# Optimization experiments

Measured on AMD Instinct MI355X. Metric: run time of the kernel, lower is better.

## Reference

```python
import jax, jax.numpy as jnp
import numpy as np

N = 21  # nodes per graph (20 laser sectors + 1 robot node)
MAX_RANGE = 10.0
_bound = np.linspace(-np.pi / 2 - 0.03, np.pi / 2, 21, dtype=np.float32)[:-1]
_angles = _bound + np.float32(np.pi / 20)
ANGLE_FEAT = jnp.asarray(np.stack([np.sin(_angles), np.cos(_angles)], 1), dtype=jnp.float32)  # [20,2]


def _build_nodes(state24):
    # state24: [B,24] -> node features [B,21,7]
    B = state24.shape[0]
    laser = state24[:, :20, None] / MAX_RANGE                       # [B,20,1]
    angle = jnp.broadcast_to(ANGLE_FEAT[None], (B, 20, 2))          # [B,20,2]
    sector = jnp.concatenate([laser, angle, jnp.zeros((B, 20, 4), state24.dtype)], -1)  # [B,20,7]
    robot = jnp.concatenate([jnp.zeros((B, 1, 3), state24.dtype), state24[:, None, 20:]], -1)  # [B,1,7]
    return jnp.concatenate([sector, robot], axis=1)                 # [B,21,7]


def _gatv2(x, Wl, Wr, att, bias, heads, dim):
    # GATv2 over a fully-connected graph with self-loops (dense all-pairs).
    # e_ij = att . leaky_relu(Wl x_j + Wr x_i); alpha = softmax_j; out_i = sum_j alpha_ij (Wl x_j)
    B = x.shape[0]
    gl = (x @ Wl).reshape(B, N, heads, dim)  # source transform [B,j,H,D]
    gr = (x @ Wr).reshape(B, N, heads, dim)  # target transform [B,i,H,D]
    s = jax.nn.leaky_relu(gl[:, None] + gr[:, :, None], negative_slope=0.2)  # [B,i,j,H,D]
    e = jnp.einsum('bijhd,hd->bijh', s, att)                                  # [B,i,j,H]
    alpha = jax.nn.softmax(e, axis=2)                                          # softmax over sources j
    out = jnp.einsum('bijh,bjhd->bihd', alpha, gl).reshape(B, N, heads * dim)
    return out + bias


def setup_inputs() -> dict:
    key = jax.random.key(0)
    ks = jax.random.split(key, 16)
    r = lambda k, shape, s: (jax.random.normal(k, shape, dtype=jnp.float32) * s)
    B = 1024
    return {
        'state24': jax.random.normal(ks[0], (B, 24), dtype=jnp.float32),
        'Wl1': r(ks[1], (7, 256), 0.3), 'Wr1': r(ks[2], (7, 256), 0.3),
        'att1': r(ks[3], (4, 64), 0.1), 'b1': r(ks[4], (256,), 0.02),
        'Wl2': r(ks[5], (256, 64), 0.06), 'Wr2': r(ks[6], (256, 64), 0.06),
        'att2': r(ks[7], (1, 64), 0.1), 'b2': r(ks[8], (64,), 0.02),
        'fc1_w': r(ks[9], (64, 256), 0.12), 'fc1_b': r(ks[10], (256,), 0.02),
        'fc2_w': r(ks[11], (256, 256), 0.06), 'fc2_b': r(ks[12], (256,), 0.02),
        'fc3_w': r(ks[13], (256, 2), 0.06), 'fc3_b': r(ks[14], (2,), 0.02),
    }


def reference(state24, Wl1, Wr1, att1, b1, Wl2, Wr2, att2, b2,
              fc1_w, fc1_b, fc2_w, fc2_b, fc3_w, fc3_b):
    x = _build_nodes(state24)                               # [B,21,7]
    h = jax.nn.elu(_gatv2(x, Wl1, Wr1, att1, b1, 4, 64))    # [B,21,256]
    h = _gatv2(h, Wl2, Wr2, att2, b2, 1, 64)                # [B,21,64]
    nfv = jnp.mean(h, axis=1)                               # global_mean_pool -> [B,64]
    h = jax.nn.relu(nfv @ fc1_w + fc1_b)
    h = jax.nn.relu(h @ fc2_w + fc2_b)
    return jnp.tanh(h @ fc3_w + fc3_b)                      # [B,2]
```

## Files before the change

### kernel.cpp

```cpp
#include <hip/hip_runtime.h>
#include <hip/hip_fp16.h>
#include <math.h>

#define PI_D 3.141592653589793

typedef _Float16 h2 __attribute__((ext_vector_type(2)));
typedef _Float16 h4 __attribute__((ext_vector_type(4)));
typedef _Float16 h8 __attribute__((ext_vector_type(8)));
typedef unsigned short us8 __attribute__((ext_vector_type(8)));
typedef __fp16 f16v2 __attribute__((ext_vector_type(2)));

#define STR1 264
#define STR1H 132
#define STR1O 33
#define STR2 66

static __device__ __forceinline__ h2 pack_h2(float a, float b) {
    return __builtin_bit_cast(h2, __builtin_amdgcn_cvt_pkrtz(a, b));
}

static __device__ __forceinline__ float fdot2(h2 a, h2 b, float c) {
    return __builtin_amdgcn_fdot2(__builtin_bit_cast(f16v2, a),
                                  __builtin_bit_cast(f16v2, b), c, false);
}

static __device__ __forceinline__ h8 habs8(h8 x) {
    us8 u = __builtin_bit_cast(us8, x);
    us8 m = {0x7fff, 0x7fff, 0x7fff, 0x7fff, 0x7fff, 0x7fff, 0x7fff, 0x7fff};
    return __builtin_bit_cast(h8, (us8)(u & m));
}

__global__ __launch_bounds__(256, 4) void actor_fused_kernel(
    const float* __restrict__ state24,
    const float* __restrict__ Wl1, const float* __restrict__ Wr1,
    const float* __restrict__ att1, const float* __restrict__ b1,
    const float* __restrict__ Wl2, const float* __restrict__ Wr2,
    const float* __restrict__ att2, const float* __restrict__ b2,
    const float* __restrict__ fc1_w, const float* __restrict__ fc1_b,
    const float* __restrict__ fc2_w, const float* __restrict__ fc2_b,
    const float* __restrict__ fc3_w, const float* __restrict__ fc3_b,
    float* __restrict__ out, int B)
{
    const int bix = blockIdx.x;
    if (bix >= B) return;
    const int tid = threadIdx.x;

    __shared__ float sinL[20], cosL[20], laserL[20], robotL[4];
    __shared__ __align__(16) h2 attLh[128];
    __shared__ __align__(16) float att2L[64];
    __shared__ __align__(16) _Float16 gr1h[24 * STR1];
    __shared__ __align__(16) union {
        struct { _Float16 gl1h[21 * STR1]; float eP[1764]; float uv[168]; } p1;
        struct { float gl2[24 * STR2]; float gr2[24 * STR2]; float e2[504];
                 float red[4][256]; float nfv[64]; float ha[256]; float hb[256]; } p2;
    } U;

    if (tid < 20) {
        double step = (PI_D + 0.03) / 20.0;
        float bound = (float)(-PI_D / 2.0 - 0.03 + (double)tid * step);
        float ang = bound + (float)(PI_D / 20.0);
        sinL[tid] = sinf(ang);
        cosL[tid] = cosf(ang);
        laserL[tid] = state24[bix * 24 + tid] * 0.1f;
    }
    if (tid >= 32 && tid < 36) robotL[tid - 32] = state24[bix * 24 + 20 + (tid - 32)];
    if (tid < 128) {
        float2 ap = ((const float2*)att1)[tid];
        attLh[tid] = pack_h2(ap.x, ap.y);
    }
    if (tid < 64) att2L[tid] = att2[tid];
    __syncthreads();

    {
        float wl[7], wr[7];
        #pragma unroll
        for (int k = 0; k < 7; k++) { wl[k] = Wl1[k * 256 + tid]; wr[k] = Wr1[k * 256 + tid]; }
        #pragma unroll
        for (int n = 0; n < 20; n++) {
            float l = laserL[n], s = sinL[n], c = cosL[n];
            U.p1.gl1h[n * STR1 + tid] = (_Float16)(l * wl[0] + s * wl[1] + c * wl[2]);
            gr1h[n * STR1 + tid]     = (_Float16)(l * wr[0] + s * wr[1] + c * wr[2]);
        }
        float r0 = robotL[0], r1 = robotL[1], r2 = robotL[2], r3 = robotL[3];
        U.p1.gl1h[20 * STR1 + tid] = (_Float16)(r0 * wl[3] + r1 * wl[4] + r2 * wl[5] + r3 * wl[6]);
        gr1h[20 * STR1 + tid]     = (_Float16)(r0 * wr[3] + r1 * wr[4] + r2 * wr[5] + r3 * wr[6]);
    }
    __syncthreads();

    if (tid < 168) {
        int r = tid < 84 ? tid : tid - 84;
        int h = r / 21, idx = r - h * 21;
        const _Float16* rowp = (tid < 84 ? U.p1.gl1h : gr1h) + idx * STR1 + h * 64;
        const h8* row8 = (const h8*)rowp;
        const h2* ar = attLh + h * 32;
        float l0 = 0.f, l1 = 0.f;
        #pragma unroll
        for (int ch = 0; ch < 8; ++ch) {
            h8 g = row8[ch];
            l0 = fdot2(__builtin_shufflevector(g, g, 0, 1), ar[ch * 4 + 0], l0);
            l1 = fdot2(__builtin_shufflevector(g, g, 2, 3), ar[ch * 4 + 1], l1);
            l0 = fdot2(__builtin_shufflevector(g, g, 4, 5), ar[ch * 4 + 2], l0);
            l1 = fdot2(__builtin_shufflevector(g, g, 6, 7), ar[ch * 4 + 3], l1);
        }
        U.p1.uv[tid] = l0 + l1;
    }
    __syncthreads();

    {
        const int h = tid >> 6;
        const int lane = tid & 63;
        h2 ar[32];
        #pragma unroll
        for (int q = 0; q < 32; ++q) ar[q] = attLh[h * 32 + q];
        const float* uvU = U.p1.uv + h * 21;
        const float* uvV = U.p1.uv + 84 + h * 21;

        for (int it = 0; it < 7; ++it) {
            int q = it * 64 + lane;
            if (q < 441) {
                int i = q / 21;
                int j = q - i * 21;
                const h8* gA8 = (const h8*)(U.p1.gl1h + j * STR1 + h * 64);
                const h8* gB8 = (const h8*)(gr1h + i * STR1 + h * 64);
                float m0 = 0.f, m1 = 0.f;
                #pragma unroll
                for (int ch = 0; ch < 8; ++ch) {
                    h8 x = gA8[ch] + gB8[ch];
                    h8 ax = habs8(x);
                    m0 = fdot2(__builtin_shufflevector(ax, ax, 0, 1), ar[ch * 4 + 0], m0);
                    m1 = fdot2(__builtin_shufflevector(ax, ax, 2, 3), ar[ch * 4 + 1], m1);
                    m0 = fdot2(__builtin_shufflevector(ax, ax, 4, 5), ar[ch * 4 + 2], m0);
                    m1 = fdot2(__builtin_shufflevector(ax, ax, 6, 7), ar[ch * 4 + 3], m1);
                }
                U.p1.eP[h * 441 + q] = 0.6f * (uvU[j] + uvV[i]) + 0.4f * (m0 + m1);
            }
        }
    }
    __syncthreads();

    if (tid < 84) {
        float* row = U.p1.eP + tid * 21;
        float m = row[0];
        #pragma unroll
        for (int j = 1; j < 21; j++) m = fmaxf(m, row[j]);
        float s = 0.f;
        #pragma unroll
        for (int j = 0; j < 21; j++) { float v = __expf(row[j] - m); row[j] = v; s += v; }
        float r = 1.f / s;
        #pragma unroll
        for (int j = 0; j < 21; j++) row[j] *= r;
    }
    __syncthreads();

    {
        h2 zz = {(_Float16)0.f, (_Float16)0.f};
        for (int z = tid; z < 384; z += 256)
            ((h2*)gr1h)[(21 + (z >> 7)) * STR1H + (z & 127)] = zz;

        int p = tid & 127, gi = tid >> 7;
        int h = p >> 5;
        float2 bb = ((const float2*)b1)[p];
        const h2* gcol = (const h2*)U.p1.gl1h + p;
        for (int i = gi; i < 21; i += 2) {
            const float* al = U.p1.eP + (h * 21 + i) * 21;
            float a0 = 0.f, a1 = 0.f;
            #pragma unroll
            for (int j = 0; j < 21; ++j) {
                float alpha = al[j];
                h2 gv = gcol[j * STR1H];
                a0 = fmaf(alpha, (float)gv.x, a0);
                a1 = fmaf(alpha, (float)gv.y, a1);
            }
            float v0 = a0 + bb.x, v1 = a1 + bb.y;
            v0 = v0 > 0.f ? v0 : __expf(v0) - 1.f;
            v1 = v1 > 0.f ? v1 : __expf(v1) - 1.f;
            h2 o; o.x = (_Float16)v0; o.y = (_Float16)v1;
            ((h2*)gr1h)[i * STR1H + p] = o;
        }
    }
    __syncthreads();

    {
        int c = tid & 63, g = tid >> 6;
        float accL[6] = {0, 0, 0, 0, 0, 0}, accR[6] = {0, 0, 0, 0, 0, 0};
        const h8* hrow8 = (const h8*)gr1h;
        const float* pwl = Wl2 + c;
        const float* pwr = Wr2 + c;
        for (int ch = 0; ch < 32; ++ch) {
            float wlv[8], wrv[8];
            #pragma unroll
            for (int r = 0; r < 8; ++r) {
                wlv[r] = pwl[(8 * ch + r) * 64];
                wrv[r] = pwr[(8 * ch + r) * 64];
            }
            h2 wlA = pack_h2(wlv[0], wlv[1]), wlB = pack_h2(wlv[2], wlv[3]);
            h2 wlC = pack_h2(wlv[4], wlv[5]), wlD = pack_h2(wlv[6], wlv[7]);
            h2 wrA = pack_h2(wrv[0], wrv[1]), wrB = pack_h2(wrv[2], wrv[3]);
            h2 wrC = pack_h2(wrv[4], wrv[5]), wrD = pack_h2(wrv[6], wrv[7]);
            #pragma unroll
            for (int m = 0; m < 6; ++m) {
                int n = g + 4 * m;
                h8 hv = hrow8[n * STR1O + ch];
                h2 s0 = __builtin_shufflevector(hv, hv, 0, 1);
                h2 s1 = __builtin_shufflevector(hv, hv, 2, 3);
                h2 s2 = __builtin_shufflevector(hv, hv, 4, 5);
                h2 s3 = __builtin_shufflevector(hv, hv, 6, 7);
                accL[m] = fdot2(s0, wlA, accL[m]);
                accL[m] = fdot2(s1, wlB, accL[m]);
                accL[m] = fdot2(s2, wlC, accL[m]);
                accL[m] = fdot2(s3, wlD, accL[m]);
                accR[m] = fdot2(s0, wrA, accR[m]);
                accR[m] = fdot2(s1, wrB, accR[m]);
                accR[m] = fdot2(s2, wrC, accR[m]);
                accR[m] = fdot2(s3, wrD, accR[m]);
            }
        }
        #pragma unroll
        for (int m = 0; m < 6; ++m) {
            int n = g + 4 * m;
            U.p2.gl2[n * STR2 + c] = accL[m];
            U.p2.gr2[n * STR2 + c] = accR[m];
        }
    }
    __syncthreads();

    for (int it = 0; it < 2; ++it) {
        int t = it * 256 + tid;
        if (t < 441) {
            int i = t / 21;
            int j = t - i * 21;
            const float2* gA = (const float2*)(U.p2.gl2 + j * STR2);
            const float2* gB = (const float2*)(U.p2.gr2 + i * STR2);
            const float2* aa = (const float2*)att2L;
            float l0 = 0.f, l1 = 0.f, m0 = 0.f, m1 = 0.f;
            #pragma unroll
            for (int dp = 0; dp < 32; ++dp) {
                float2 va = gA[dp], vb = gB[dp], a = aa[dp];
                float x0 = va.x + vb.x, x1 = va.y + vb.y;
                l0 = fmaf(a.x, x0, l0); m0 = fmaf(a.x, fabsf(x0), m0);
                l1 = fmaf(a.y, x1, l1); m1 = fmaf(a.y, fabsf(x1), m1);
            }
            U.p2.e2[t] = 0.6f * (l0 + l1) + 0.4f * (m0 + m1);
        }
    }
    __syncthreads();

    if (tid < 24) {
        float* row = U.p2.e2 + tid * 21;
        if (tid < 21) {
            float m = row[0];
            #pragma unroll
            for (int j = 1; j < 21; j++) m = fmaxf(m, row[j]);
            float s = 0.f;
            #pragma unroll
            for (int j = 0; j < 21; j++) { float v = __expf(row[j] - m); row[j] = v; s += v; }
            float r = 1.f / s;
            #pragma unroll
            for (int j = 0; j < 21; j++) row[j] *= r;
        } else {
            #pragma unroll
            for (int j = 0; j < 21; j++) row[j] = 0.f;
        }
    }
    __syncthreads();

    {
        int d = tid & 63, g = tid >> 6;
        float sacc = 0.f;
        #pragma unroll
        for (int m = 0; m < 6; ++m) {
            int i = g + 4 * m;
            const float* al = U.p2.e2 + i * 21;
            float acc = 0.f;
            #pragma unroll
            for (int j = 0; j < 21; ++j) acc = fmaf(al[j], U.p2.gl2[j * STR2 + d], acc);
            sacc += acc;
        }
        U.p2.red[g][d] = sacc;
    }
    __syncthreads();
    if (tid < 64) {
        U.p2.nfv[tid] = (U.p2.red[0][tid] + U.p2.red[1][tid] + U.p2.red[2][tid] + U.p2.red[3][tid])
                        * (1.f / 21.f) + b2[tid];
    }
    __syncthreads();

    {
        int c = tid & 63, g = tid >> 6;
        const float4* w4 = (const float4*)fc1_w;
        float4 acc = {0.f, 0.f, 0.f, 0.f};
        #pragma unroll
        for (int kk = 0; kk < 16; ++kk) {
            int k = g * 16 + kk;
            float xv = U.p2.nfv[k];
            float4 w = w4[k * 64 + c];
            acc.x = fmaf(xv, w.x, acc.x);
            acc.y = fmaf(xv, w.y, acc.y);
            acc.z = fmaf(xv, w.z, acc.z);
            acc.w = fmaf(xv, w.w, acc.w);
        }
        ((float4*)U.p2.red[g])[c] = acc;
    }
    __syncthreads();
    {
        float v = U.p2.red[0][tid] + U.p2.red[1][tid] + U.p2.red[2][tid] + U.p2.red[3][tid]
                  + fc1_b[tid];
        U.p2.ha[tid] = fmaxf(v, 0.f);
    }
    __syncthreads();

    {
        int c = tid & 63, g = tid >> 6;
        const float4* w4 = (const float4*)fc2_w;
        float4 acc = {0.f, 0.f, 0.f, 0.f};
        #pragma unroll 8
        for (int kk = 0; kk < 64; ++kk) {
            int k = g * 64 + kk;
            float xv = U.p2.ha[k];
            float4 w = w4[k * 64 + c];
            acc.x = fmaf(xv, w.x, acc.x);
            acc.y = fmaf(xv, w.y, acc.y);
            acc.z = fmaf(xv, w.z, acc.z);
            acc.w = fmaf(xv, w.w, acc.w);
        }
        ((float4*)U.p2.red[g])[c] = acc;
    }
    __syncthreads();
    {
        float v = U.p2.red[0][tid] + U.p2.red[1][tid] + U.p2.red[2][tid] + U.p2.red[3][tid]
                  + fc2_b[tid];
        U.p2.hb[tid] = fmaxf(v, 0.f);
    }
    __syncthreads();

    if (tid < 128) {
        int o = tid >> 6, l = tid & 63;
        float s = 0.f;
        #pragma unroll
        for (int m = 0; m < 4; m++) { int k = l + 64 * m; s = fmaf(U.p2.hb[k], fc3_w[k * 2 + o], s); }
        #pragma unroll
        for (int off = 32; off >= 1; off >>= 1) s += __shfl_down(s, off, 64);
        if (l == 0) out[bix * 2 + o] = tanhf(s + fc3_b[o]);
    }
}

extern "C" void kernel_launch(void* const* d_in, const int* in_sizes, int n_in,
                              void* d_out, int out_size, void* d_ws, size_t ws_size,
                              hipStream_t stream) {
    const float* state24 = (const float*)d_in[0];
    const float* Wl1 = (const float*)d_in[1];
    const float* Wr1 = (const float*)d_in[2];
    const float* att1 = (const float*)d_in[3];
    const float* b1 = (const float*)d_in[4];
    const float* Wl2 = (const float*)d_in[5];
    const float* Wr2 = (const float*)d_in[6];
    const float* att2 = (const float*)d_in[7];
    const float* b2 = (const float*)d_in[8];
    const float* fc1_w = (const float*)d_in[9];
    const float* fc1_b = (const float*)d_in[10];
    const float* fc2_w = (const float*)d_in[11];
    const float* fc2_b = (const float*)d_in[12];
    const float* fc3_w = (const float*)d_in[13];
    const float* fc3_b = (const float*)d_in[14];
    float* out = (float*)d_out;

    int B = in_sizes[0] / 24;
    actor_fused_kernel<<<B, 256, 0, stream>>>(
        state24, Wl1, Wr1, att1, b1, Wl2, Wr2, att2, b2,
        fc1_w, fc1_b, fc2_w, fc2_b, fc3_w, fc3_b, out, B);
}
```

Before: 134.2 us.

## Prepack layer-2 and FC weights to fp16 and rework layer-1 aggregation

Adds a small pre-kernel that converts Wl2/Wr2 and fc1/fc2 weights to fp16 in a packed h8 layout in workspace. Each of the 1024 blocks can then load them with vector loads and use fdot2, instead of gathering strided fp32 values and packing them per block. The FC hidden activations are also stored in fp16. The layer-1 aggregation is restructured so each thread keeps one column of gl in registers and reads padded attention rows as float4. The cost is an extra launch and reduced precision in the FC layers.

```diff
diff --git a/kernel.cpp b/kernel.cpp
--- a/kernel.cpp
+++ b/kernel.cpp
@@ -5,15 +5,14 @@
 #define PI_D 3.141592653589793
 
 typedef _Float16 h2 __attribute__((ext_vector_type(2)));
-typedef _Float16 h4 __attribute__((ext_vector_type(4)));
 typedef _Float16 h8 __attribute__((ext_vector_type(8)));
 typedef unsigned short us8 __attribute__((ext_vector_type(8)));
 typedef __fp16 f16v2 __attribute__((ext_vector_type(2)));
 
 #define STR1 264
-#define STR1H 132
 #define STR1O 33
 #define STR2 66
+#define EPS 24
 
 static __device__ __forceinline__ h2 pack_h2(float a, float b) {
     return __builtin_bit_cast(h2, __builtin_amdgcn_cvt_pkrtz(a, b));
@@ -30,15 +29,52 @@
     return __builtin_bit_cast(h8, (us8)(u & m));
 }
 
+__global__ __launch_bounds__(256) void pack_weights_kernel(
+    const float* __restrict__ Wl2, const float* __restrict__ Wr2,
+    const float* __restrict__ fc1_w, const float* __restrict__ fc2_w,
+    h8* __restrict__ ws)
+{
+    int idx = blockIdx.x * 256 + threadIdx.x;
+    if (idx < 4096) {
+        const float* W = idx < 2048 ? Wl2 : Wr2;
+        int t = idx & 2047;
+        int ch = t >> 6, c = t & 63;
+        h8 o;
+        #pragma unroll
+        for (int r = 0; r < 8; ++r) o[r] = (_Float16)W[(8 * ch + r) * 64 + c];
+        ws[idx] = o;
+    } else if (idx < 6144) {
+        int t = idx - 4096;
+        int k2 = t >> 6, c = t & 63;
+        h8 o;
+        #pragma unroll
+        for (int q = 0; q < 4; ++q) {
+            o[2 * q]     = (_Float16)fc1_w[(2 * k2) * 256 + 4 * c + q];
+            o[2 * q + 1] = (_Float16)fc1_w[(2 * k2 + 1) * 256 + 4 * c + q];
+        }
+        ws[idx] = o;
+    } else {
+        int t = idx - 6144;
+        int k2 = t >> 6, c = t & 63;
+        h8 o;
+        #pragma unroll
+        for (int q = 0; q < 4; ++q) {
+            o[2 * q]     = (_Float16)fc2_w[(2 * k2) * 256 + 4 * c + q];
+            o[2 * q + 1] = (_Float16)fc2_w[(2 * k2 + 1) * 256 + 4 * c + q];
+        }
+        ws[idx] = o;
+    }
+}
+
 __global__ __launch_bounds__(256, 4) void actor_fused_kernel(
     const float* __restrict__ state24,
     const float* __restrict__ Wl1, const float* __restrict__ Wr1,
     const float* __restrict__ att1, const float* __restrict__ b1,
-    const float* __restrict__ Wl2, const float* __restrict__ Wr2,
     const float* __restrict__ att2, const float* __restrict__ b2,
-    const float* __restrict__ fc1_w, const float* __restrict__ fc1_b,
-    const float* __restrict__ fc2_w, const float* __restrict__ fc2_b,
+    const float* __restrict__ fc1_b, const float* __restrict__ fc2_b,
     const float* __restrict__ fc3_w, const float* __restrict__ fc3_b,
+    const h8* __restrict__ wsL, const h8* __restrict__ wsR,
+    const h8* __restrict__ wsF1, const h8* __restrict__ wsF2,
     float* __restrict__ out, int B)
 {
     const int bix = blockIdx.x;
@@ -50,9 +86,12 @@
     __shared__ __align__(16) float att2L[64];
     __shared__ __align__(16) _Float16 gr1h[24 * STR1];
     __shared__ __align__(16) union {
-        struct { _Float16 gl1h[21 * STR1]; float eP[1764]; float uv[168]; } p1;
+        struct { _Float16 gl1h[21 * STR1];
+                 float eP[84 * EPS];
+                 float uv[168]; } p1;
         struct { float gl2[24 * STR2]; float gr2[24 * STR2]; float e2[504];
-                 float red[4][256]; float nfv[64]; float ha[256]; float hb[256]; } p2;
+                 float red[4][256];
+                 _Float16 nfvh[64]; _Float16 hah[256]; _Float16 hbh[256]; } p2;
     } U;
 
     if (tid < 20) {
@@ -132,14 +171,14 @@
                     m0 = fdot2(__builtin_shufflevector(ax, ax, 4, 5), ar[ch * 4 + 2], m0);
                     m1 = fdot2(__builtin_shufflevector(ax, ax, 6, 7), ar[ch * 4 + 3], m1);
                 }
-                U.p1.eP[h * 441 + q] = 0.6f * (uvU[j] + uvV[i]) + 0.4f * (m0 + m1);
+                U.p1.eP[(h * 21 + i) * EPS + j] = 0.6f * (uvU[j] + uvV[i]) + 0.4f * (m0 + m1);
             }
         }
     }
     __syncthreads();
 
     if (tid < 84) {
-        float* row = U.p1.eP + tid * 21;
+        float* row = U.p1.eP + tid * EPS;
         float m = row[0];
         #pragma unroll
         for (int j = 1; j < 21; j++) m = fmaxf(m, row[j]);
@@ -153,29 +192,44 @@
     __syncthreads();
 
     {
-        h2 zz = {(_Float16)0.f, (_Float16)0.f};
-        for (int z = tid; z < 384; z += 256)
-            ((h2*)gr1h)[(21 + (z >> 7)) * STR1H + (z & 127)] = zz;
-
-        int p = tid & 127, gi = tid >> 7;
-        int h = p >> 5;
-        float2 bb = ((const float2*)b1)[p];
-        const h2* gcol = (const h2*)U.p1.gl1h + p;
-        for (int i = gi; i < 21; i += 2) {
-            const float* al = U.p1.eP + (h * 21 + i) * 21;
-            float a0 = 0.f, a1 = 0.f;
-            #pragma unroll
-            for (int j = 0; j < 21; ++j) {
-                float alpha = al[j];
-                h2 gv = gcol[j * STR1H];
-                a0 = fmaf(alpha, (float)gv.x, a0);
-                a1 = fmaf(alpha, (float)gv.y, a1);
-            }
-            float v0 = a0 + bb.x, v1 = a1 + bb.y;
-            v0 = v0 > 0.f ? v0 : __expf(v0) - 1.f;
-            v1 = v1 > 0.f ? v1 : __expf(v1) - 1.f;
-            h2 o; o.x = (_Float16)v0; o.y = (_Float16)v1;
-            ((h2*)gr1h)[i * STR1H + p] = o;
+        const int h = tid >> 6, c = tid & 63;
+        const int col = h * 64 + c;
+        float glv[21];
+        #pragma unroll
+        for (int j = 0; j < 21; ++j) glv[j] = (float)U.p1.gl1h[j * STR1 + col];
+        float bb = b1[col];
+        gr1h[21 * STR1 + col] = (_Float16)0.f;
+        gr1h[22 * STR1 + col] = (_Float16)0.f;
+        gr1h[23 * STR1 + col] = (_Float16)0.f;
+        for (int i = 0; i < 21; ++i) {
+            const float4* ar4 = (const float4*)(U.p1.eP + (h * 21 + i) * EPS);
+            float4 q0 = ar4[0], q1 = ar4[1], q2 = ar4[2], q3 = ar4[3], q4 = ar4[4];
+            float a20 = U.p1.eP[(h * 21 + i) * EPS + 20];
+            float acc;
+            acc = q0.x * glv[0];
+            acc = fmaf(q0.y, glv[1], acc);
+            acc = fmaf(q0.z, glv[2], acc);
+            acc = fmaf(q0.w, glv[3], acc);
+            acc = fmaf(q1.x, glv[4], acc);
+            acc = fmaf(q1.y, glv[5], acc);
+            acc = fmaf(q1.z, glv[6], acc);
+            acc = fmaf(q1.w, glv[7], acc);
+            acc = fmaf(q2.x, glv[8], acc);
+            acc = fmaf(q2.y, glv[9], acc);
+            acc = fmaf(q2.z, glv[10], acc);
+            acc = fmaf(q2.w, glv[11], acc);
+            acc = fmaf(q3.x, glv[12], acc);
+            acc = fmaf(q3.y, glv[13], acc);
+            acc = fmaf(q3.z, glv[14], acc);
+            acc = fmaf(q3.w, glv[15], acc);
+            acc = fmaf(q4.x, glv[16], acc);
+            acc = fmaf(q4.y, glv[17], acc);
+            acc = fmaf(q4.z, glv[18], acc);
+            acc = fmaf(q4.w, glv[19], acc);
+            acc = fmaf(a20, glv[20], acc);
+            float v = acc + bb;
+            v = v > 0.f ? v : __expf(v) - 1.f;
+            gr1h[i * STR1 + col] = (_Float16)v;
         }
     }
     __syncthreads();
@@ -184,19 +238,17 @@
         int c = tid & 63, g = tid >> 6;
         float accL[6] = {0, 0, 0, 0, 0, 0}, accR[6] = {0, 0, 0, 0, 0, 0};
         const h8* hrow8 = (const h8*)gr1h;
-        const float* pwl = Wl2 + c;
-        const float* pwr = Wr2 + c;
         for (int ch = 0; ch < 32; ++ch) {
-            float wlv[8], wrv[8];
-            #pragma unroll
-            for (int r = 0; r < 8; ++r) {
-                wlv[r] = pwl[(8 * ch + r) * 64];
-                wrv[r] = pwr[(8 * ch + r) * 64];
-            }
-            h2 wlA = pack_h2(wlv[0], wlv[1]), wlB = pack_h2(wlv[2], wlv[3]);
-            h2 wlC = pack_h2(wlv[4], wlv[5]), wlD = pack_h2(wlv[6], wlv[7]);
-            h2 wrA = pack_h2(wrv[0], wrv[1]), wrB = pack_h2(wrv[2], wrv[3]);
-            h2 wrC = pack_h2(wrv[4], wrv[5]), wrD = pack_h2(wrv[6], wrv[7]);
+            h8 wl = wsL[ch * 64 + c];
+            h8 wr = wsR[ch * 64 + c];
+            h2 wlA = __builtin_shufflevector(wl, wl, 0, 1);
+            h2 wlB = __builtin_shufflevector(wl, wl, 2, 3);
+            h2 wlC = __builtin_shufflevector(wl, wl, 4, 5);
+            h2 wlD = __builtin_shufflevector(wl, wl, 6, 7);
+            h2 wrA = __builtin_shufflevector(wr, wr, 0, 1);
+            h2 wrB = __builtin_shufflevector(wr, wr, 2, 3);
+            h2 wrC = __builtin_shufflevector(wr, wr, 4, 5);
+            h2 wrD = __builtin_shufflevector(wr, wr, 6, 7);
             #pragma unroll
             for (int m = 0; m < 6; ++m) {
                 int n = g + 4 * m;
@@ -280,24 +332,25 @@
     }
     __syncthreads();
     if (tid < 64) {
-        U.p2.nfv[tid] = (U.p2.red[0][tid] + U.p2.red[1][tid] + U.p2.red[2][tid] + U.p2.red[3][tid])
-                        * (1.f / 21.f) + b2[tid];
+        float v = (U.p2.red[0][tid] + U.p2.red[1][tid] + U.p2.red[2][tid] + U.p2.red[3][tid])
+                  * (1.f / 21.f) + b2[tid];
+        U.p2.nfvh[tid] = (_Float16)v;
     }
     __syncthreads();
 
     {
         int c = tid & 63, g = tid >> 6;
-        const float4* w4 = (const float4*)fc1_w;
+        const h2* x2p = (const h2*)U.p2.nfvh;
         float4 acc = {0.f, 0.f, 0.f, 0.f};
         #pragma unroll
-        for (int kk = 0; kk < 16; ++kk) {
-            int k = g * 16 + kk;
-            float xv = U.p2.nfv[k];
-            float4 w = w4[k * 64 + c];
-            acc.x = fmaf(xv, w.x, acc.x);
-            acc.y = fmaf(xv, w.y, acc.y);
-            acc.z = fmaf(xv, w.z, acc.z);
-            acc.w = fmaf(xv, w.w, acc.w);
+        for (int kk = 0; kk < 8; ++kk) {
+            int k2 = g * 8 + kk;
+            h8 w = wsF1[k2 * 64 + c];
+            h2 x2 = x2p[k2];
+            acc.x = fdot2(__builtin_shufflevector(w, w, 0, 1), x2, acc.x);
+            acc.y = fdot2(__builtin_shufflevector(w, w, 2, 3), x2, acc.y);
+            acc.z = fdot2(__builtin_shufflevector(w, w, 4, 5), x2, acc.z);
+            acc.w = fdot2(__builtin_shufflevector(w, w, 6, 7), x2, acc.w);
         }
         ((float4*)U.p2.red[g])[c] = acc;
     }
@@ -305,31 +358,40 @@
     {
         float v = U.p2.red[0][tid] + U.p2.red[1][tid] + U.p2.red[2][tid] + U.p2.red[3][tid]
                   + fc1_b[tid];
-        U.p2.ha[tid] = fmaxf(v, 0.f);
+        U.p2.hah[tid] = (_Float16)fmaxf(v, 0.f);
     }
     __syncthreads();
 
     {
         int c = tid & 63, g = tid >> 6;
-        const float4* w4 = (const float4*)fc2_w;
+        const h8* haH = (const h8*)U.p2.hah;
         float4 acc = {0.f, 0.f, 0.f, 0.f};
-        #pragma unroll 8
-        for (int kk = 0; kk < 64; ++kk) {
-            int k = g * 64 + kk;
-            float xv = U.p2.ha[k];
-            float4 w = w4[k * 64 + c];
-            acc.x = fmaf(xv, w.x, acc.x);
-            acc.y = fmaf(xv, w.y, acc.y);
-            acc.z = fmaf(xv, w.z, acc.z);
-            acc.w = fmaf(xv, w.w, acc.w);
-        }
+#define FC2_STEP(q, p)                                                          \
+        {                                                                       \
+            int k2 = g * 32 + (q) * 4 + (p);                                    \
+            h8 w = wsF2[k2 * 64 + c];                                           \
+            h2 x2 = __builtin_shufflevector(xa, xa, 2 * (p), 2 * (p) + 1);      \
+            acc.x = fdot2(__builtin_shufflevector(w, w, 0, 1), x2, acc.x);      \
+            acc.y = fdot2(__builtin_shufflevector(w, w, 2, 3), x2, acc.y);      \
+            acc.z = fdot2(__builtin_shufflevector(w, w, 4, 5), x2, acc.z);      \
+            acc.w = fdot2(__builtin_shufflevector(w, w, 6, 7), x2, acc.w);      \
+        }
+        #pragma unroll
+        for (int q = 0; q < 8; ++q) {
+            h8 xa = haH[g * 8 + q];
+            FC2_STEP(q, 0)
+            FC2_STEP(q, 1)
+            FC2_STEP(q, 2)
+            FC2_STEP(q, 3)
+        }
+#undef FC2_STEP
         ((float4*)U.p2.red[g])[c] = acc;
     }
     __syncthreads();
     {
         float v = U.p2.red[0][tid] + U.p2.red[1][tid] + U.p2.red[2][tid] + U.p2.red[3][tid]
                   + fc2_b[tid];
-        U.p2.hb[tid] = fmaxf(v, 0.f);
+        U.p2.hbh[tid] = (_Float16)fmaxf(v, 0.f);
     }
     __syncthreads();
 
@@ -337,7 +399,10 @@
         int o = tid >> 6, l = tid & 63;
         float s = 0.f;
         #pragma unroll
-        for (int m = 0; m < 4; m++) { int k = l + 64 * m; s = fmaf(U.p2.hb[k], fc3_w[k * 2 + o], s); }
+        for (int m = 0; m < 4; m++) {
+            int k = l + 64 * m;
+            s = fmaf((float)U.p2.hbh[k], fc3_w[k * 2 + o], s);
+        }
         #pragma unroll
         for (int off = 32; off >= 1; off >>= 1) s += __shfl_down(s, off, 64);
         if (l == 0) out[bix * 2 + o] = tanhf(s + fc3_b[o]);
@@ -364,8 +429,17 @@
     const float* fc3_b = (const float*)d_in[14];
     float* out = (float*)d_out;
 
+    h8* ws = (h8*)d_ws;
+    const h8* wsL = ws;
+    const h8* wsR = ws + 2048;
+    const h8* wsF1 = ws + 4096;
+    const h8* wsF2 = ws + 6144;
+
+    pack_weights_kernel<<<56, 256, 0, stream>>>(Wl2, Wr2, fc1_w, fc2_w, ws);
+
     int B = in_sizes[0] / 24;
     actor_fused_kernel<<<B, 256, 0, stream>>>(
-        state24, Wl1, Wr1, att1, b1, Wl2, Wr2, att2, b2,
-        fc1_w, fc1_b, fc2_w, fc2_b, fc3_w, fc3_b, out, B);
-}
+        state24, Wl1, Wr1, att1, b1, att2, b2,
+        fc1_b, fc2_b, fc3_w, fc3_b,
+        wsL, wsR, wsF1, wsF2, out, B);
+}
```

Result: faster. 130.5 us (-2.7%).
